# Optimization experiments

Measured on AMD Instinct MI355X. Metric: run time of the kernel, lower is better.

Reference implementation:

```python
import jax, jax.numpy as jnp
import numpy as np

H = 6  # hidden size == input size

def _lstm_layer(x_tbf, h0, c0, Wih, Whh, bih, bhh):
    # x_tbf: [T, B, F]; Wih: [4H, F]; Whh: [4H, H]; biases: [4H]
    b = bih + bhh
    def step(carry, xt):
        h, c = carry
        gates = xt @ Wih.T + h @ Whh.T + b  # [B, 4H]
        i, f, g, o = jnp.split(gates, 4, axis=-1)  # PyTorch gate order i,f,g,o
        i = jax.nn.sigmoid(i)
        f = jax.nn.sigmoid(f)
        g = jnp.tanh(g)
        o = jax.nn.sigmoid(o)
        c = f * c + i * g
        h = o * jnp.tanh(c)
        return (h, c), h
    (_, _), hs = jax.lax.scan(step, (h0, c0), x_tbf)
    return hs  # [T, B, H]

def setup_inputs() -> dict:
    key = jax.random.key(0)
    ks = jax.random.split(key, 9)
    B, T = 4096, 1024
    s = 1.0 / np.sqrt(H)  # PyTorch LSTM init: U(-1/sqrt(H), 1/sqrt(H))
    u = lambda k, shape: jax.random.uniform(k, shape, jnp.float32, -s, s)
    return {
        "x": jax.random.normal(ks[0], (B, T, 6), jnp.float32),
        "w_ih_l0": u(ks[1], (4 * H, 6)),
        "w_hh_l0": u(ks[2], (4 * H, H)),
        "b_ih_l0": u(ks[3], (4 * H,)),
        "b_hh_l0": u(ks[4], (4 * H,)),
        "w_ih_l1": u(ks[5], (4 * H, H)),
        "w_hh_l1": u(ks[6], (4 * H, H)),
        "b_ih_l1": u(ks[7], (4 * H,)),
        "b_hh_l1": u(ks[8], (4 * H,)),
    }

def reference(x, w_ih_l0, w_hh_l0, b_ih_l0, b_hh_l0, w_ih_l1, w_hh_l1, b_ih_l1, b_hh_l1):
    B = x.shape[0]
    x_t = jnp.transpose(x, (1, 0, 2))  # [T, B, 6]
    z = jnp.zeros((B, H), x.dtype)
    h1 = _lstm_layer(x_t, z, z, w_ih_l0, w_hh_l0, b_ih_l0, b_hh_l0)
    h2 = _lstm_layer(h1, z, z, w_ih_l1, w_hh_l1, b_ih_l1, b_hh_l1)
    return jnp.transpose(h2, (1, 0, 2))  # [B, T, H] (x[0] of nn.LSTM output)
```

## Files before the change

### kernel.cpp

```cpp
#include <hip/hip_runtime.h>

#define T_STEPS 1024

__device__ __forceinline__ float vexp2(float x) { return __builtin_amdgcn_exp2f(x); }
__device__ __forceinline__ float vrcp(float x)  { return __builtin_amdgcn_rcpf(x); }
__device__ __forceinline__ float sigm(float x) {
    return vrcp(1.0f + vexp2(x * -1.44269504088896340736f));
}
__device__ __forceinline__ float tanh_f(float x) {
    return fmaf(2.0f, sigm(2.0f * x), -1.0f);
}

#define SWZ(v, s) \
    __int_as_float(__builtin_amdgcn_ds_swizzle(__float_as_int(v), (((s) << 5) | 0x10)))

__device__ __forceinline__ float cell_step(
    const float xb[6], const float h0b[6], const float h1b[6], float& c,
    const float wai[6], const float waf[6], const float wag[6], const float wao[6],
    const float wbi[6], const float wbf[6], const float wbg[6], const float wbo[6],
    float bI, float bF, float bG, float bO, bool isL1)
{
    float bin[6];
#pragma unroll
    for (int q = 0; q < 6; ++q) bin[q] = isL1 ? h1b[q] : xb[q];

    float gI = bI, gF = bF, gG = bG, gO = bO;
    float hI = 0.f, hF = 0.f, hG = 0.f, hO = 0.f;
#pragma unroll
    for (int q = 0; q < 6; ++q) {
        gF = fmaf(wbf[q], bin[q], gF);
        gI = fmaf(wbi[q], bin[q], gI);
        gG = fmaf(wbg[q], bin[q], gG);
        gO = fmaf(wbo[q], bin[q], gO);
        hF = fmaf(waf[q], h0b[q], hF);
        hI = fmaf(wai[q], h0b[q], hI);
        hG = fmaf(wag[q], h0b[q], hG);
        hO = fmaf(wao[q], h0b[q], hO);
    }
    float aF = sigm(gF + hF);
    float aI = sigm(gI + hI);
    float aG = tanh_f(gG + hG);
    c = fmaf(aF, c, aI * aG);
    float aO = sigm(gO + hO);
    return aO * tanh_f(c);
}

__global__ __launch_bounds__(256) void lstm2_kernel(
    const float* __restrict__ x,
    const float* __restrict__ wih0, const float* __restrict__ whh0,
    const float* __restrict__ bih0, const float* __restrict__ bhh0,
    const float* __restrict__ wih1, const float* __restrict__ whh1,
    const float* __restrict__ bih1, const float* __restrict__ bhh1,
    float* __restrict__ out, int Btot)
{
    const int tid = threadIdx.x;
    const int grp = tid >> 4;
    const int l   = tid & 15;
    const int b   = blockIdx.x * 16 + grp;
    if (b >= Btot) return;

    const bool isL1 = (l & 8) != 0;
    int j = l & 7; if (j > 5) j = 5;

    const float* wa  = isL1 ? wih1 : whh0;
    const float* wb  = isL1 ? whh1 : wih0;
    const float* bip = isL1 ? bih1 : bih0;
    const float* bhp = isL1 ? bhh1 : bhh0;

    float wai[6], waf[6], wag[6], wao[6];
    float wbi[6], wbf[6], wbg[6], wbo[6];
#pragma unroll
    for (int k = 0; k < 6; ++k) {
        wai[k] = wa[(j     ) * 6 + k];
        waf[k] = wa[(6 + j ) * 6 + k];
        wag[k] = wa[(12 + j) * 6 + k];
        wao[k] = wa[(18 + j) * 6 + k];
        wbi[k] = wb[(j     ) * 6 + k];
        wbf[k] = wb[(6 + j ) * 6 + k];
        wbg[k] = wb[(12 + j) * 6 + k];
        wbo[k] = wb[(18 + j) * 6 + k];
    }
    const float bI = bip[j]      + bhp[j];
    const float bF = bip[6 + j]  + bhp[6 + j];
    const float bG = bip[12 + j] + bhp[12 + j];
    const float bO = bip[18 + j] + bhp[18 + j];

    float h0b[6], h1b[6];
#pragma unroll
    for (int k = 0; k < 6; ++k) { h0b[k] = 0.0f; h1b[k] = 0.0f; }
    float c = 0.0f;

    const float* px = x + (size_t)b * (T_STEPS * 6);
    float* ps = out + (size_t)b * (T_STEPS * 6) + (isL1 ? (l - 8) : 0);
    const bool lstore = (l >= 8) && (l < 14);

    auto loadx = [&](int t, float v[6]) {
        const float2* p2 = reinterpret_cast<const float2*>(px + (size_t)t * 6);
        float2 a = p2[0], b2 = p2[1], c2 = p2[2];
        v[0] = a.x; v[1] = a.y; v[2] = b2.x; v[3] = b2.y; v[4] = c2.x; v[5] = c2.y;
    };

#define ITER(K, CUR, PF)                                                       \
    {                                                                          \
        int tn_ = (K) + 3; if (tn_ > T_STEPS - 1) tn_ = T_STEPS - 1;           \
        loadx(tn_, PF);                                                        \
        float hv = cell_step(CUR, h0b, h1b, c, wai, waf, wag, wao,             \
                             wbi, wbf, wbg, wbo, bI, bF, bG, bO, isL1);        \
        if ((K) >= 1 && lstore) ps[(size_t)((K) - 1) * 6] = hv;                \
        h0b[0] = SWZ(hv, 0);  h0b[1] = SWZ(hv, 1);  h0b[2] = SWZ(hv, 2);       \
        h0b[3] = SWZ(hv, 3);  h0b[4] = SWZ(hv, 4);  h0b[5] = SWZ(hv, 5);       \
        h1b[0] = SWZ(hv, 8);  h1b[1] = SWZ(hv, 9);  h1b[2] = SWZ(hv, 10);      \
        h1b[3] = SWZ(hv, 11); h1b[4] = SWZ(hv, 12); h1b[5] = SWZ(hv, 13);      \
    }

    float xA[6], xB[6], xC[6], xD[6];
    loadx(0, xA); loadx(1, xB); loadx(2, xC);

    ITER(0, xA, xD);
    if (isL1) c = 0.0f;
#pragma unroll
    for (int k = 0; k < 6; ++k) h1b[k] = 0.0f;

    for (int k = 1; k <= T_STEPS; k += 4) {
        ITER(k,     xB, xA);
        ITER(k + 1, xC, xB);
        ITER(k + 2, xD, xC);
        ITER(k + 3, xA, xD);
    }
#undef ITER
}

extern "C" void kernel_launch(void* const* d_in, const int* in_sizes, int n_in,
                              void* d_out, int out_size, void* d_ws, size_t ws_size,
                              hipStream_t stream)
{
    const float* x    = (const float*)d_in[0];
    const float* wih0 = (const float*)d_in[1];
    const float* whh0 = (const float*)d_in[2];
    const float* bih0 = (const float*)d_in[3];
    const float* bhh0 = (const float*)d_in[4];
    const float* wih1 = (const float*)d_in[5];
    const float* whh1 = (const float*)d_in[6];
    const float* bih1 = (const float*)d_in[7];
    const float* bhh1 = (const float*)d_in[8];
    float* out = (float*)d_out;

    const int Btot   = in_sizes[0] / (T_STEPS * 6);
    const int blocks = (Btot + 15) / 16;
    hipLaunchKernelGGL(lstm2_kernel, dim3(blocks), dim3(256), 0, stream,
                       x, wih0, whh0, bih0, bhh0, wih1, whh1, bih1, bhh1, out, Btot);
}
```

Baseline: 425.6 us.

## Split LSTM gates across two lane halves per batch with xor-8 swizzle exchange

Each batch row now uses 32 lanes instead of 16. Lanes with bit 3 set compute the g and o gates, the others compute i and f, and the two halves swap activations through an xor-8 ds_swizzle. This halves the FMAs and transcendental calls per lane on the serial recurrence path. The cost is twice as many threads per row, so half as many rows per block, plus extra swizzles and per-lane selects.

```diff
diff --git a/kernel.cpp b/kernel.cpp
--- a/kernel.cpp
+++ b/kernel.cpp
@@ -11,39 +11,10 @@
     return fmaf(2.0f, sigm(2.0f * x), -1.0f);
 }
 
-#define SWZ(v, s) \
-    __int_as_float(__builtin_amdgcn_ds_swizzle(__float_as_int(v), (((s) << 5) | 0x10)))
-
-__device__ __forceinline__ float cell_step(
-    const float xb[6], const float h0b[6], const float h1b[6], float& c,
-    const float wai[6], const float waf[6], const float wag[6], const float wao[6],
-    const float wbi[6], const float wbf[6], const float wbg[6], const float wbo[6],
-    float bI, float bF, float bG, float bO, bool isL1)
-{
-    float bin[6];
-#pragma unroll
-    for (int q = 0; q < 6; ++q) bin[q] = isL1 ? h1b[q] : xb[q];
-
-    float gI = bI, gF = bF, gG = bG, gO = bO;
-    float hI = 0.f, hF = 0.f, hG = 0.f, hO = 0.f;
-#pragma unroll
-    for (int q = 0; q < 6; ++q) {
-        gF = fmaf(wbf[q], bin[q], gF);
-        gI = fmaf(wbi[q], bin[q], gI);
-        gG = fmaf(wbg[q], bin[q], gG);
-        gO = fmaf(wbo[q], bin[q], gO);
-        hF = fmaf(waf[q], h0b[q], hF);
-        hI = fmaf(wai[q], h0b[q], hI);
-        hG = fmaf(wag[q], h0b[q], hG);
-        hO = fmaf(wao[q], h0b[q], hO);
-    }
-    float aF = sigm(gF + hF);
-    float aI = sigm(gI + hI);
-    float aG = tanh_f(gG + hG);
-    c = fmaf(aF, c, aI * aG);
-    float aO = sigm(gO + hO);
-    return aO * tanh_f(c);
-}
+#define SWZ_BCAST(v, s) \
+    __int_as_float(__builtin_amdgcn_ds_swizzle(__float_as_int(v), ((s) << 5)))
+#define SWZ_XOR8(v) \
+    __int_as_float(__builtin_amdgcn_ds_swizzle(__float_as_int(v), ((8 << 10) | 0x1F)))
 
 __global__ __launch_bounds__(256) void lstm2_kernel(
     const float* __restrict__ x,
@@ -54,36 +25,30 @@
     float* __restrict__ out, int Btot)
 {
     const int tid = threadIdx.x;
-    const int grp = tid >> 4;
-    const int l   = tid & 15;
-    const int b   = blockIdx.x * 16 + grp;
+    const int l   = tid & 31;
+    const int b   = blockIdx.x * 8 + (tid >> 5);
     if (b >= Btot) return;
 
-    const bool isL1 = (l & 8) != 0;
+    const bool isL1 = (l & 16) != 0;
+    const bool isGO = (l & 8) != 0;
     int j = l & 7; if (j > 5) j = 5;
+
+    const int rA = isGO ? (12 + j) : j;
+    const int rB = isGO ? (18 + j) : (6 + j);
 
     const float* wa  = isL1 ? wih1 : whh0;
     const float* wb  = isL1 ? whh1 : wih0;
     const float* bip = isL1 ? bih1 : bih0;
     const float* bhp = isL1 ? bhh1 : bhh0;
 
-    float wai[6], waf[6], wag[6], wao[6];
-    float wbi[6], wbf[6], wbg[6], wbo[6];
+    float waA[6], waB[6], wbA[6], wbB[6];
 #pragma unroll
     for (int k = 0; k < 6; ++k) {
-        wai[k] = wa[(j     ) * 6 + k];
-        waf[k] = wa[(6 + j ) * 6 + k];
-        wag[k] = wa[(12 + j) * 6 + k];
-        wao[k] = wa[(18 + j) * 6 + k];
-        wbi[k] = wb[(j     ) * 6 + k];
-        wbf[k] = wb[(6 + j ) * 6 + k];
-        wbg[k] = wb[(12 + j) * 6 + k];
-        wbo[k] = wb[(18 + j) * 6 + k];
+        waA[k] = wa[rA * 6 + k]; waB[k] = wa[rB * 6 + k];
+        wbA[k] = wb[rA * 6 + k]; wbB[k] = wb[rB * 6 + k];
     }
-    const float bI = bip[j]      + bhp[j];
-    const float bF = bip[6 + j]  + bhp[6 + j];
-    const float bG = bip[12 + j] + bhp[12 + j];
-    const float bO = bip[18 + j] + bhp[18 + j];
+    const float bA = bip[rA] + bhp[rA];
+    const float bB = bip[rB] + bhp[rB];
 
     float h0b[6], h1b[6];
 #pragma unroll
@@ -91,8 +56,8 @@
     float c = 0.0f;
 
     const float* px = x + (size_t)b * (T_STEPS * 6);
-    float* ps = out + (size_t)b * (T_STEPS * 6) + (isL1 ? (l - 8) : 0);
-    const bool lstore = (l >= 8) && (l < 14);
+    float* ps = out + (size_t)b * (T_STEPS * 6) + (l - 16);
+    const bool lstore = (l >= 16) && (l < 22);
 
     auto loadx = [&](int t, float v[6]) {
         const float2* p2 = reinterpret_cast<const float2*>(px + (size_t)t * 6);
@@ -100,17 +65,33 @@
         v[0] = a.x; v[1] = a.y; v[2] = b2.x; v[3] = b2.y; v[4] = c2.x; v[5] = c2.y;
     };
 
-#define ITER(K, CUR, PF)                                                       \
-    {                                                                          \
-        int tn_ = (K) + 3; if (tn_ > T_STEPS - 1) tn_ = T_STEPS - 1;           \
-        loadx(tn_, PF);                                                        \
-        float hv = cell_step(CUR, h0b, h1b, c, wai, waf, wag, wao,             \
-                             wbi, wbf, wbg, wbo, bI, bF, bG, bO, isL1);        \
-        if ((K) >= 1 && lstore) ps[(size_t)((K) - 1) * 6] = hv;                \
-        h0b[0] = SWZ(hv, 0);  h0b[1] = SWZ(hv, 1);  h0b[2] = SWZ(hv, 2);       \
-        h0b[3] = SWZ(hv, 3);  h0b[4] = SWZ(hv, 4);  h0b[5] = SWZ(hv, 5);       \
-        h1b[0] = SWZ(hv, 8);  h1b[1] = SWZ(hv, 9);  h1b[2] = SWZ(hv, 10);      \
-        h1b[3] = SWZ(hv, 11); h1b[4] = SWZ(hv, 12); h1b[5] = SWZ(hv, 13);      \
+#define ITER(K, CUR, PF)                                                        \
+    {                                                                           \
+        int tn_ = (K) + 3; if (tn_ > T_STEPS - 1) tn_ = T_STEPS - 1;            \
+        loadx(tn_, PF);                                                         \
+        float gA = bA, gB = bB, hA = 0.0f, hB = 0.0f;                           \
+        _Pragma("unroll")                                                       \
+        for (int q = 0; q < 6; ++q) {                                           \
+            float bin = isL1 ? h1b[q] : CUR[q];                                 \
+            gA = fmaf(wbA[q], bin, gA);  gB = fmaf(wbB[q], bin, gB);            \
+            hA = fmaf(waA[q], h0b[q], hA); hB = fmaf(waB[q], h0b[q], hB);       \
+        }                                                                       \
+        float sA = gA + hA, sB = gB + hB;                                       \
+        float preA = isGO ? 2.0f * sA : sA;                                     \
+        float tAct = sigm(preA);                                                \
+        float aA = isGO ? fmaf(2.0f, tAct, -1.0f) : tAct;   \
+        float aB = sigm(sB);                                 \
+        float eA = SWZ_XOR8(aA);         \
+        float eB = SWZ_XOR8(aB);         \
+        c = fmaf(aB, c, aA * eA);                        \
+        float hv = eB * tanh_f(c);                       \
+        if ((K) >= 1 && lstore) ps[(size_t)((K) - 1) * 6] = hv;                 \
+        h0b[0] = SWZ_BCAST(hv, 0);  h0b[1] = SWZ_BCAST(hv, 1);                  \
+        h0b[2] = SWZ_BCAST(hv, 2);  h0b[3] = SWZ_BCAST(hv, 3);                  \
+        h0b[4] = SWZ_BCAST(hv, 4);  h0b[5] = SWZ_BCAST(hv, 5);                  \
+        h1b[0] = SWZ_BCAST(hv, 16); h1b[1] = SWZ_BCAST(hv, 17);                 \
+        h1b[2] = SWZ_BCAST(hv, 18); h1b[3] = SWZ_BCAST(hv, 19);                 \
+        h1b[4] = SWZ_BCAST(hv, 20); h1b[5] = SWZ_BCAST(hv, 21);                 \
     }
 
     float xA[6], xB[6], xC[6], xD[6];
@@ -146,7 +127,7 @@
     float* out = (float*)d_out;
 
     const int Btot   = in_sizes[0] / (T_STEPS * 6);
-    const int blocks = (Btot + 15) / 16;
+    const int blocks = (Btot + 7) / 8;
     hipLaunchKernelGGL(lstm2_kernel, dim3(blocks), dim3(256), 0, stream,
                        x, wih0, whh0, bih0, bhh0, wih1, whh1, bih1, bhh1, out, Btot);
 }
```

New measurement: 450.3 us. +5.8%, slower.
